# Optimization experiments

Measured on AMD Instinct MI355X. Metric: run time of the kernel, lower is better.

## Reference

```python
import jax, jax.numpy as jnp
import numpy as np

B, S, D, E, H, SL = 4, 2048, 2048, 16, 1024, 1
NUM_SLOTS = E * SL
TEMP = 1.0
TOP_K = 2
EPS = 1e-8


def setup_inputs() -> dict:
    key = jax.random.key(0)
    k0, k1, k2, k3 = jax.random.split(key, 4)
    x = jax.random.normal(k0, (B, S, D), dtype=jnp.float32)
    Wd = jax.random.normal(k1, (NUM_SLOTS, D), dtype=jnp.float32) * 0.02
    W1 = jax.random.normal(k2, (E, D, H), dtype=jnp.float32) * 0.02
    b1 = jnp.zeros((E, H), dtype=jnp.float32)
    W2 = jax.random.normal(k3, (E, H, D), dtype=jnp.float32) * 0.02
    b2 = jnp.zeros((E, D), dtype=jnp.float32)
    return {"x": x, "Wd": Wd, "W1": W1, "b1": b1, "W2": W2, "b2": b2}


def reference(x, Wd, W1, b1, W2, b2):
    lead = x.shape[:-1]
    xf = x.reshape(-1, D)                      # [T, D]
    T = xf.shape[0]

    logits = (xf @ Wd.T) / TEMP                # [T, num_slots]
    dispatch = jax.nn.softmax(logits, axis=0)  # softmax over tokens
    combine = jax.nn.softmax(logits, axis=-1)  # softmax over slots

    # Aggregate tokens into slots, run all experts as one batched GEMM chain.
    slot_in = (dispatch.T @ xf).reshape(E, SL, D)                    # [E, SL, D]
    h = jax.nn.gelu(jnp.einsum('esd,edh->esh', slot_in, W1) + b1[:, None, :],
                    approximate=False)
    slot_out = (jnp.einsum('esh,ehd->esd', h, W2) + b2[:, None, :]).reshape(NUM_SLOTS, D)

    out = (combine @ slot_out).reshape(x.shape)

    # Router stats / losses (eval mode: no EMA update of train_scores).
    expert_weights = combine.reshape(T, E, SL).mean(-1)              # [T, E]
    mean_usage = expert_weights.mean(0)                              # [E]
    p = jax.nn.softmax(Wd.mean(0).reshape(E, -1).mean(-1))
    router_loss = E * jnp.sum(mean_usage * p)

    topk_w, topk_idx = jax.lax.top_k(expert_weights, TOP_K)
    topk_w_norm = topk_w / jnp.clip(topk_w.sum(-1, keepdims=True), EPS)

    gate_weights = expert_weights.reshape(*lead, E)
    routing_entropy = -(gate_weights * jnp.log(gate_weights + EPS)).sum(-1).mean()

    return (out,
            router_loss,
            gate_weights,
            topk_idx.reshape(*lead, TOP_K),
            topk_w_norm.reshape(*lead, TOP_K),
            mean_usage,
            routing_entropy,
            dispatch.reshape(*lead, NUM_SLOTS))
```

## Files before the change

kernel.cpp:

```cpp
#include <hip/hip_runtime.h>
#include <math.h>

#define TTOK 8192
#define DIM  2048
#define NH   1024

#define OFF_PART1   0u
#define OFF_NUM     2097152u
#define OFF_COMBINE 2228224u
#define OFF_CSUM    2359296u
#define OFF_MUSUM   2361344u
#define OFF_ENT     2363392u
#define OFF_PART6   2363520u
#define OFF_SRAW    10752128u
#define OFF_HBUF    10784896u
#define OFF_SLOT    10801280u

#define O_OUT   0u
#define O_LOSS  16777216u
#define O_GATE  16777217u
#define O_TOPI  16908289u
#define O_TOPW  16924673u
#define O_MU    16941057u
#define O_ENTR  16941073u
#define O_DISP  16941074u

__device__ __forceinline__ float wave_sum(float v){
  #pragma unroll
  for (int o=1;o<64;o<<=1) v += __shfl_xor(v,o,64);
  return v;
}

__global__ __launch_bounds__(256) void ka_logits(const float* __restrict__ x,
                                                 const float* __restrict__ Wd,
                                                 float* __restrict__ part1){
  const int tb = blockIdx.x >> 4;
  const int kc = blockIdx.x & 15;
  const int t  = tb*256 + threadIdx.x;
  const float4* __restrict__ xr = (const float4*)(x + (size_t)t*DIM + kc*128);
  float acc[16];
  #pragma unroll
  for (int e=0;e<16;e++) acc[e]=0.f;
  #pragma unroll 4
  for (int k4=0;k4<32;k4++){
    float4 xv = xr[k4];
    #pragma unroll
    for (int e=0;e<16;e++){
      float4 w = *(const float4*)(Wd + e*DIM + kc*128 + k4*4);
      acc[e] += xv.x*w.x + xv.y*w.y + xv.z*w.z + xv.w*w.w;
    }
  }
  float4* po = (float4*)(part1 + ((size_t)kc*TTOK + t)*16);
  po[0] = make_float4(acc[0],acc[1],acc[2],acc[3]);
  po[1] = make_float4(acc[4],acc[5],acc[6],acc[7]);
  po[2] = make_float4(acc[8],acc[9],acc[10],acc[11]);
  po[3] = make_float4(acc[12],acc[13],acc[14],acc[15]);
}

__global__ __launch_bounds__(256) void kb_router(const float* __restrict__ part1,
    float* __restrict__ num, float* __restrict__ csum_part,
    float* __restrict__ combine, float* __restrict__ gate_out,
    float* __restrict__ topi_out, float* __restrict__ topw_out,
    float* __restrict__ musum_part, float* __restrict__ ent_part){
  const int tid = threadIdx.x;
  const int i = blockIdx.x*256 + tid;
  const float4* p1 = (const float4*)part1;
  float4 s = make_float4(0,0,0,0);
  #pragma unroll
  for (int kc=0;kc<16;kc++){
    float4 v = p1[(size_t)kc*32768 + i];
    s.x+=v.x; s.y+=v.y; s.z+=v.z; s.w+=v.w;
  }
  float4 n4 = make_float4(expf(s.x),expf(s.y),expf(s.z),expf(s.w));
  ((float4*)num)[i] = n4;
  __shared__ float Lg[64][20];
  const int tl = tid>>2, q = tid&3;
  *(float4*)(&Lg[tl][q*4]) = s;
  float4 n = n4;
  #pragma unroll
  for (int o=4;o<64;o<<=1){
    n.x += __shfl_xor(n.x,o,64); n.y += __shfl_xor(n.y,o,64);
    n.z += __shfl_xor(n.z,o,64); n.w += __shfl_xor(n.w,o,64);
  }
  __shared__ float4 red[4][4];
  const int w = tid>>6, lane = tid&63;
  if (lane<4) red[w][lane] = n;
  __syncthreads();
  if (tid<4){
    float4 a=red[0][tid],b=red[1][tid],c=red[2][tid],d=red[3][tid];
    *(float4*)(csum_part + blockIdx.x*16 + tid*4) =
      make_float4(a.x+b.x+c.x+d.x, a.y+b.y+c.y+d.y, a.z+b.z+c.z+d.z, a.w+b.w+c.w+d.w);
  }
  if (tid < 64){
    const int gt = blockIdx.x*64 + tid;
    float l[16];
    #pragma unroll
    for (int e=0;e<16;e++) l[e] = Lg[tid][e];
    float m = l[0];
    #pragma unroll
    for (int e=1;e<16;e++) m = fmaxf(m,l[e]);
    float c[16]; float sm=0.f;
    #pragma unroll
    for (int e=0;e<16;e++){ c[e]=expf(l[e]-m); sm+=c[e]; }
    float inv = 1.f/sm;
    #pragma unroll
    for (int e=0;e<16;e++) c[e]*=inv;
    float4* co = (float4*)(combine + (size_t)gt*16);
    co[0]=make_float4(c[0],c[1],c[2],c[3]);   co[1]=make_float4(c[4],c[5],c[6],c[7]);
    co[2]=make_float4(c[8],c[9],c[10],c[11]); co[3]=make_float4(c[12],c[13],c[14],c[15]);
    float* go = gate_out + (size_t)gt*16;
    #pragma unroll
    for (int e=0;e<16;e++) go[e]=c[e];
    float v0=-1.f, v1=-1.f; int i0=0, i1=0;
    #pragma unroll
    for (int e=0;e<16;e++){
      float ce=c[e];
      if (ce>v0){ v1=v0; i1=i0; v0=ce; i0=e; }
      else if (ce>v1){ v1=ce; i1=e; }
    }
    float dn = fmaxf(v0+v1, 1e-8f);
    topi_out[(size_t)gt*2+0]=(float)i0; topi_out[(size_t)gt*2+1]=(float)i1;
    topw_out[(size_t)gt*2+0]=v0/dn;     topw_out[(size_t)gt*2+1]=v1/dn;
    float ent=0.f;
    #pragma unroll
    for (int e=0;e<16;e++) ent -= c[e]*logf(c[e]+1e-8f);
    #pragma unroll
    for (int e=0;e<16;e++){
      float v = wave_sum(c[e]);
      if (tid==0) musum_part[blockIdx.x*16+e] = v;
    }
    float ve = wave_sum(ent);
    if (tid==0) ent_part[blockIdx.x] = ve;
  }
}

__global__ __launch_bounds__(256) void kd_slotin(const float* __restrict__ x,
    const float* __restrict__ num, const float* __restrict__ csum_part,
    const float* __restrict__ musum_part, const float* __restrict__ ent_part,
    const float* __restrict__ Wd,
    float* __restrict__ part6, float* __restrict__ disp_out,
    float* __restrict__ loss_out, float* __restrict__ mu_out, float* __restrict__ ent_out){
  const int tc = blockIdx.x >> 1;
  const int dc = blockIdx.x & 1;
  const int tid = threadIdx.x;
  const int d  = dc*1024 + tid*4;
  const int t0 = tc*32;
  __shared__ float4 sN[128];
  if (tid < 128) sN[tid] = ((const float4*)num)[t0*4 + tid];
  __syncthreads();
  float4 acc[16];
  #pragma unroll
  for (int e=0;e<16;e++) acc[e]=make_float4(0,0,0,0);
  #pragma unroll 2
  for (int t=0;t<32;t++){
    const float4 xv = *(const float4*)(x + (size_t)(t0+t)*DIM + d);
    #pragma unroll
    for (int qq=0;qq<4;qq++){
      float4 nq = sN[t*4+qq];
      acc[qq*4+0].x=fmaf(nq.x,xv.x,acc[qq*4+0].x); acc[qq*4+0].y=fmaf(nq.x,xv.y,acc[qq*4+0].y);
      acc[qq*4+0].z=fmaf(nq.x,xv.z,acc[qq*4+0].z); acc[qq*4+0].w=fmaf(nq.x,xv.w,acc[qq*4+0].w);
      acc[qq*4+1].x=fmaf(nq.y,xv.x,acc[qq*4+1].x); acc[qq*4+1].y=fmaf(nq.y,xv.y,acc[qq*4+1].y);
      acc[qq*4+1].z=fmaf(nq.y,xv.z,acc[qq*4+1].z); acc[qq*4+1].w=fmaf(nq.y,xv.w,acc[qq*4+1].w);
      acc[qq*4+2].x=fmaf(nq.z,xv.x,acc[qq*4+2].x); acc[qq*4+2].y=fmaf(nq.z,xv.y,acc[qq*4+2].y);
      acc[qq*4+2].z=fmaf(nq.z,xv.z,acc[qq*4+2].z); acc[qq*4+2].w=fmaf(nq.z,xv.w,acc[qq*4+2].w);
      acc[qq*4+3].x=fmaf(nq.w,xv.x,acc[qq*4+3].x); acc[qq*4+3].y=fmaf(nq.w,xv.y,acc[qq*4+3].y);
      acc[qq*4+3].z=fmaf(nq.w,xv.z,acc[qq*4+3].z); acc[qq*4+3].w=fmaf(nq.w,xv.w,acc[qq*4+3].w);
    }
  }
  #pragma unroll
  for (int e=0;e<16;e++)
    *(float4*)(part6 + ((size_t)tc*16+e)*DIM + d) = acc[e];

  if (dc==0){
    __shared__ float sIv[16][16];
    __shared__ float sInv[16];
    { int g = tid>>4, e = tid&15;
      float v=0.f;
      #pragma unroll
      for (int k=0;k<8;k++) v += csum_part[(g*8+k)*16 + e];
      sIv[g][e]=v; }
    __syncthreads();
    if (tid<16){
      float v=0.f;
      #pragma unroll
      for (int g2=0;g2<16;g2++) v+=sIv[g2][tid];
      sInv[tid]=1.f/v;
    }
    __syncthreads();
    const float* sNf = (const float*)sN;
    const int j = tid*2;
    float2 dv = make_float2(sNf[j]*sInv[j&15], sNf[j+1]*sInv[(j+1)&15]);
    *(float2*)(disp_out + (size_t)t0*16 + j) = dv;

    if (tc==0){
      __shared__ float sq[16][16];
      __shared__ float smu[16];
      __shared__ float sqv[16];
      __shared__ float sqe[16];
      {
        int s = tid>>4, ch = tid&15;
        const float* base = Wd + (size_t)s*DIM + ch*128;
        float qv=0.f;
        for (int ii=0;ii<128;ii+=4){ float4 v=*(const float4*)(base+ii); qv+=v.x+v.y+v.z+v.w; }
        sq[s][ch]=qv;
      }
      if (tid<16){
        float mu=0.f;
        for (int b=0;b<128;b++) mu += musum_part[b*16+tid];
        mu/=8192.f;
        mu_out[tid]=mu; smu[tid]=mu;
      }
      if (tid==32){ float es=0.f; for(int b=0;b<128;b++) es+=ent_part[b]; ent_out[0]=es/8192.f; }
      __syncthreads();
      if (tid<16){ float qv=0.f; for(int s=0;s<16;s++) qv+=sq[s][tid]; sqv[tid]=qv/2048.f; }
      __syncthreads();
      if (tid<16){
        float qm=-INFINITY;
        for (int e=0;e<16;e++) qm=fmaxf(qm,sqv[e]);
        sqe[tid]=expf(sqv[tid]-qm);
      }
      __syncthreads();
      if (tid==0){
        float qs=0.f; for(int e=0;e<16;e++) qs+=sqe[e];
        float loss=0.f; for(int e=0;e<16;e++) loss+=smu[e]*(sqe[e]/qs);
        loss_out[0]=16.f*loss;
      }
    }
  }
}

__global__ __launch_bounds__(256) void ke_sraw(const float* __restrict__ part6,
    float* __restrict__ sraw){
  const int tid = threadIdx.x;
  const int half = tid>>7, il = tid&127;
  const int i = blockIdx.x*128 + il;
  float s=0.f;
  #pragma unroll 8
  for (int tc=half*128; tc<half*128+128; tc++) s += part6[(size_t)tc*32768 + i];
  __shared__ float s2[256];
  s2[tid]=s;
  __syncthreads();
  if (tid<128){
    int ii = blockIdx.x*128 + tid;
    sraw[ii] = s2[tid]+s2[tid+128];
  }
}

__global__ __launch_bounds__(256) void kf_h(const float* __restrict__ sraw,
    const float* __restrict__ W1, const float* __restrict__ b1,
    const float* __restrict__ csum_part, float* __restrict__ hbuf){
  const int e  = blockIdx.x >> 5;
  const int hc = blockIdx.x & 31;
  const int hbase = hc*32;
  const int tid = threadIdx.x;
  __shared__ float sr[2048];
  __shared__ float sacc[256];
  __shared__ float sIpart[2];
  { const float4* s4 = (const float4*)(sraw + (size_t)e*DIM);
    float4 a = s4[tid*2], b = s4[tid*2+1];
    *(float4*)(&sr[tid*8]) = a; *(float4*)(&sr[tid*8+4]) = b; }
  if (tid < 128){
    float v = csum_part[tid*16 + e];
    #pragma unroll
    for (int o=1;o<64;o<<=1) v += __shfl_xor(v,o,64);
    if ((tid&63)==0) sIpart[tid>>6] = v;
  }
  __syncthreads();
  const int hl = tid&31, ds = tid>>5;
  float acc = 0.f;
  const float* wp = W1 + (size_t)e*DIM*NH + hbase + hl;
  #pragma unroll 16
  for (int d2=0; d2<256; d2++){
    const int dd = d2*8 + ds;
    acc = fmaf(sr[dd], wp[(size_t)dd*NH], acc);
  }
  sacc[tid] = acc;
  __syncthreads();
  if (tid < 32){
    float s = 0.f;
    #pragma unroll
    for (int k=0;k<8;k++) s += sacc[k*32 + tid];
    float invs = 1.f/(sIpart[0]+sIpart[1]);
    float pre = invs*s + b1[(size_t)e*NH + hbase + tid];
    hbuf[(size_t)e*NH + hbase + tid] = 0.5f*pre*(1.f+erff(pre*0.70710678118654752f));
  }
}

__global__ __launch_bounds__(256) void kg_so(const float* __restrict__ hbuf,
    const float* __restrict__ W2, const float* __restrict__ b2,
    float* __restrict__ slot_out){
  const int e  = blockIdx.x >> 5;
  const int dc = blockIdx.x & 31;
  const int dbase = dc*64;
  const int tid = threadIdx.x;
  __shared__ float hh[1024];
  __shared__ float sacc[256];
  { const float4* h4 = (const float4*)(hbuf + (size_t)e*NH);
    *(float4*)(&hh[tid*4]) = h4[tid]; }
  __syncthreads();
  const int dl = tid&63, hs = tid>>6;
  float acc = 0.f;
  const float* wp = W2 + (size_t)e*NH*DIM + dbase + dl;
  #pragma unroll 16
  for (int h2=0; h2<256; h2++){
    const int hidx = h2*4 + hs;
    acc = fmaf(hh[hidx], wp[(size_t)hidx*DIM], acc);
  }
  sacc[tid] = acc;
  __syncthreads();
  if (tid < 64){
    float s = sacc[tid] + sacc[64+tid] + sacc[128+tid] + sacc[192+tid];
    slot_out[(size_t)e*DIM + dbase + tid] = s + b2[(size_t)e*DIM + dbase + tid];
  }
}

__global__ __launch_bounds__(256) void kh_out(const float* __restrict__ slot_out,
    const float* __restrict__ combine, float* __restrict__ out){
  const int tb = blockIdx.x >> 1;
  const int dc = blockIdx.x & 1;
  const int t0 = tb*16;
  const int d  = dc*1024 + threadIdx.x*4;
  float4 sv[16];
  #pragma unroll
  for (int e=0;e<16;e++) sv[e] = *(const float4*)(slot_out + (size_t)e*DIM + d);
  #pragma unroll 2
  for (int t=0;t<16;t++){
    const float* cr = combine + (size_t)(t0+t)*16;
    float4 a = make_float4(0,0,0,0);
    #pragma unroll
    for (int e=0;e<16;e++){
      float c = cr[e];
      a.x=fmaf(c,sv[e].x,a.x); a.y=fmaf(c,sv[e].y,a.y);
      a.z=fmaf(c,sv[e].z,a.z); a.w=fmaf(c,sv[e].w,a.w);
    }
    *(float4*)(out + (size_t)(t0+t)*DIM + d) = a;
  }
}

extern "C" void kernel_launch(void* const* d_in, const int* in_sizes, int n_in,
                              void* d_out, int out_size, void* d_ws, size_t ws_size,
                              hipStream_t stream) {
  const float* x  = (const float*)d_in[0];
  const float* Wd = (const float*)d_in[1];
  const float* W1 = (const float*)d_in[2];
  const float* b1 = (const float*)d_in[3];
  const float* W2 = (const float*)d_in[4];
  const float* b2 = (const float*)d_in[5];
  float* out = (float*)d_out;
  float* ws  = (float*)d_ws;

  float* part1   = ws + OFF_PART1;
  float* num     = ws + OFF_NUM;
  float* combine = ws + OFF_COMBINE;
  float* csump   = ws + OFF_CSUM;
  float* musump  = ws + OFF_MUSUM;
  float* entp    = ws + OFF_ENT;
  float* part6   = ws + OFF_PART6;
  float* sraw    = ws + OFF_SRAW;
  float* hbuf    = ws + OFF_HBUF;
  float* slot_out= ws + OFF_SLOT;

  ka_logits<<<512, 256, 0, stream>>>(x, Wd, part1);
  kb_router<<<128, 256, 0, stream>>>(part1, num, csump, combine, out + O_GATE,
                                     out + O_TOPI, out + O_TOPW, musump, entp);
  kd_slotin<<<512, 256, 0, stream>>>(x, num, csump, musump, entp, Wd,
                                     part6, out + O_DISP, out + O_LOSS,
                                     out + O_MU, out + O_ENTR);
  ke_sraw<<<256, 256, 0, stream>>>(part6, sraw);
  kf_h<<<512, 256, 0, stream>>>(sraw, W1, b1, csump, hbuf);
  kg_so<<<512, 256, 0, stream>>>(hbuf, W2, b2, slot_out);
  kh_out<<<1024, 256, 0, stream>>>(slot_out, combine, out + O_OUT);
}
```

Before: 179.2 us.

## Repartition logits, W1 and W2 GEMV kernels into finer splits with more blocks

The logits kernel now splits the reduction dimension into 64 chunks of 32 and has each thread handle two tokens, which reuses each Wd load twice. The router now sums 64 partials instead of 16. The two expert GEMV kernels double their block counts by narrowing the column tile and switching to contiguous per-thread row ranges. The workspace is laid out again so that part1, which has grown to 64 partials, reuses the part6 region. The aim is more parallelism for the memory-bound GEMVs. The cost is more partial-sum traffic and less coalesced column access for the narrower tiles.

New measurement: 203.8 us. 13.7% more time.

```diff
diff --git a/kernel.cpp b/kernel.cpp
--- a/kernel.cpp
+++ b/kernel.cpp
@@ -6,15 +6,15 @@
 #define NH   1024
 
 #define OFF_PART1   0u
-#define OFF_NUM     2097152u
-#define OFF_COMBINE 2228224u
-#define OFF_CSUM    2359296u
-#define OFF_MUSUM   2361344u
-#define OFF_ENT     2363392u
-#define OFF_PART6   2363520u
-#define OFF_SRAW    10752128u
-#define OFF_HBUF    10784896u
-#define OFF_SLOT    10801280u
+#define OFF_PART6   0u
+#define OFF_NUM     8388608u
+#define OFF_COMBINE 8519680u
+#define OFF_CSUM    8650752u
+#define OFF_MUSUM   8652800u
+#define OFF_ENT     8654848u
+#define OFF_SRAW    8654976u
+#define OFF_HBUF    8687744u
+#define OFF_SLOT    8704128u
 
 #define O_OUT   0u
 #define O_LOSS  16777216u
@@ -34,27 +34,31 @@
 __global__ __launch_bounds__(256) void ka_logits(const float* __restrict__ x,
                                                  const float* __restrict__ Wd,
                                                  float* __restrict__ part1){
-  const int tb = blockIdx.x >> 4;
-  const int kc = blockIdx.x & 15;
-  const int t  = tb*256 + threadIdx.x;
-  const float4* __restrict__ xr = (const float4*)(x + (size_t)t*DIM + kc*128);
-  float acc[16];
-  #pragma unroll
-  for (int e=0;e<16;e++) acc[e]=0.f;
-  #pragma unroll 4
-  for (int k4=0;k4<32;k4++){
-    float4 xv = xr[k4];
+  const int tb = blockIdx.x >> 6;
+  const int kc = blockIdx.x & 63;
+  const int t0 = tb*512 + threadIdx.x;
+  const float4* __restrict__ xr0 = (const float4*)(x + (size_t)t0*DIM + kc*32);
+  const float4* __restrict__ xr1 = (const float4*)(x + (size_t)(t0+256)*DIM + kc*32);
+  float a0[16], a1[16];
+  #pragma unroll
+  for (int e=0;e<16;e++){ a0[e]=0.f; a1[e]=0.f; }
+  #pragma unroll
+  for (int k4=0;k4<8;k4++){
+    float4 x0 = xr0[k4];
+    float4 x1 = xr1[k4];
     #pragma unroll
     for (int e=0;e<16;e++){
-      float4 w = *(const float4*)(Wd + e*DIM + kc*128 + k4*4);
-      acc[e] += xv.x*w.x + xv.y*w.y + xv.z*w.z + xv.w*w.w;
-    }
-  }
-  float4* po = (float4*)(part1 + ((size_t)kc*TTOK + t)*16);
-  po[0] = make_float4(acc[0],acc[1],acc[2],acc[3]);
-  po[1] = make_float4(acc[4],acc[5],acc[6],acc[7]);
-  po[2] = make_float4(acc[8],acc[9],acc[10],acc[11]);
-  po[3] = make_float4(acc[12],acc[13],acc[14],acc[15]);
+      float4 w = *(const float4*)(Wd + e*DIM + kc*32 + k4*4);
+      a0[e] += x0.x*w.x + x0.y*w.y + x0.z*w.z + x0.w*w.w;
+      a1[e] += x1.x*w.x + x1.y*w.y + x1.z*w.z + x1.w*w.w;
+    }
+  }
+  float4* p0 = (float4*)(part1 + ((size_t)kc*TTOK + t0)*16);
+  p0[0]=make_float4(a0[0],a0[1],a0[2],a0[3]);   p0[1]=make_float4(a0[4],a0[5],a0[6],a0[7]);
+  p0[2]=make_float4(a0[8],a0[9],a0[10],a0[11]); p0[3]=make_float4(a0[12],a0[13],a0[14],a0[15]);
+  float4* p1 = (float4*)(part1 + ((size_t)kc*TTOK + t0+256)*16);
+  p1[0]=make_float4(a1[0],a1[1],a1[2],a1[3]);   p1[1]=make_float4(a1[4],a1[5],a1[6],a1[7]);
+  p1[2]=make_float4(a1[8],a1[9],a1[10],a1[11]); p1[3]=make_float4(a1[12],a1[13],a1[14],a1[15]);
 }
 
 __global__ __launch_bounds__(256) void kb_router(const float* __restrict__ part1,
@@ -66,8 +70,8 @@
   const int i = blockIdx.x*256 + tid;
   const float4* p1 = (const float4*)part1;
   float4 s = make_float4(0,0,0,0);
-  #pragma unroll
-  for (int kc=0;kc<16;kc++){
+  #pragma unroll 8
+  for (int kc=0;kc<64;kc++){
     float4 v = p1[(size_t)kc*32768 + i];
     s.x+=v.x; s.y+=v.y; s.z+=v.z; s.w+=v.w;
   }
@@ -249,9 +253,9 @@
 __global__ __launch_bounds__(256) void kf_h(const float* __restrict__ sraw,
     const float* __restrict__ W1, const float* __restrict__ b1,
     const float* __restrict__ csum_part, float* __restrict__ hbuf){
-  const int e  = blockIdx.x >> 5;
-  const int hc = blockIdx.x & 31;
-  const int hbase = hc*32;
+  const int e  = blockIdx.x >> 6;
+  const int hc = blockIdx.x & 63;
+  const int hbase = hc*16;
   const int tid = threadIdx.x;
   __shared__ float sr[2048];
   __shared__ float sacc[256];
@@ -266,20 +270,20 @@
     if ((tid&63)==0) sIpart[tid>>6] = v;
   }
   __syncthreads();
-  const int hl = tid&31, ds = tid>>5;
+  const int hl = tid&15, ds = tid>>4;
   float acc = 0.f;
   const float* wp = W1 + (size_t)e*DIM*NH + hbase + hl;
   #pragma unroll 16
-  for (int d2=0; d2<256; d2++){
-    const int dd = d2*8 + ds;
+  for (int i=0;i<128;i++){
+    const int dd = ds*128 + i;
     acc = fmaf(sr[dd], wp[(size_t)dd*NH], acc);
   }
   sacc[tid] = acc;
   __syncthreads();
-  if (tid < 32){
+  if (tid < 16){
     float s = 0.f;
     #pragma unroll
-    for (int k=0;k<8;k++) s += sacc[k*32 + tid];
+    for (int k=0;k<16;k++) s += sacc[k*16 + tid];
     float invs = 1.f/(sIpart[0]+sIpart[1]);
     float pre = invs*s + b1[(size_t)e*NH + hbase + tid];
     hbuf[(size_t)e*NH + hbase + tid] = 0.5f*pre*(1.f+erff(pre*0.70710678118654752f));
@@ -289,27 +293,29 @@
 __global__ __launch_bounds__(256) void kg_so(const float* __restrict__ hbuf,
     const float* __restrict__ W2, const float* __restrict__ b2,
     float* __restrict__ slot_out){
-  const int e  = blockIdx.x >> 5;
-  const int dc = blockIdx.x & 31;
-  const int dbase = dc*64;
+  const int e  = blockIdx.x >> 6;
+  const int dc = blockIdx.x & 63;
+  const int dbase = dc*32;
   const int tid = threadIdx.x;
   __shared__ float hh[1024];
   __shared__ float sacc[256];
   { const float4* h4 = (const float4*)(hbuf + (size_t)e*NH);
     *(float4*)(&hh[tid*4]) = h4[tid]; }
   __syncthreads();
-  const int dl = tid&63, hs = tid>>6;
+  const int dl = tid&31, hs = tid>>5;
   float acc = 0.f;
   const float* wp = W2 + (size_t)e*NH*DIM + dbase + dl;
   #pragma unroll 16
-  for (int h2=0; h2<256; h2++){
-    const int hidx = h2*4 + hs;
+  for (int i=0;i<128;i++){
+    const int hidx = hs*128 + i;
     acc = fmaf(hh[hidx], wp[(size_t)hidx*DIM], acc);
   }
   sacc[tid] = acc;
   __syncthreads();
-  if (tid < 64){
-    float s = sacc[tid] + sacc[64+tid] + sacc[128+tid] + sacc[192+tid];
+  if (tid < 32){
+    float s = 0.f;
+    #pragma unroll
+    for (int k=0;k<8;k++) s += sacc[k*32 + tid];
     slot_out[(size_t)e*DIM + dbase + tid] = s + b2[(size_t)e*DIM + dbase + tid];
   }
 }
@@ -360,14 +366,14 @@
   float* hbuf    = ws + OFF_HBUF;
   float* slot_out= ws + OFF_SLOT;
 
-  ka_logits<<<512, 256, 0, stream>>>(x, Wd, part1);
+  ka_logits<<<1024, 256, 0, stream>>>(x, Wd, part1);
   kb_router<<<128, 256, 0, stream>>>(part1, num, csump, combine, out + O_GATE,
                                      out + O_TOPI, out + O_TOPW, musump, entp);
   kd_slotin<<<512, 256, 0, stream>>>(x, num, csump, musump, entp, Wd,
                                      part6, out + O_DISP, out + O_LOSS,
                                      out + O_MU, out + O_ENTR);
   ke_sraw<<<256, 256, 0, stream>>>(part6, sraw);
-  kf_h<<<512, 256, 0, stream>>>(sraw, W1, b1, csump, hbuf);
-  kg_so<<<512, 256, 0, stream>>>(hbuf, W2, b2, slot_out);
+  kf_h<<<1024, 256, 0, stream>>>(sraw, W1, b1, csump, hbuf);
+  kg_so<<<1024, 256, 0, stream>>>(hbuf, W2, b2, slot_out);
   kh_out<<<1024, 256, 0, stream>>>(slot_out, combine, out + O_OUT);
 }
```

## Fuse logits, router, and slot aggregation into one kernel; merge reductions

Applied to the files above, without the earlier changes.

Merges the logits GEMV, the router softmax/top-k/entropy, and the token-to-slot aggregation into a single 512-thread kernel per 32-token chunk. Each x row is then read while it is likely still in cache, and the part1 partial-logit buffer round trip goes away. The part6 reduction is merged with the dispatch normalisation, loss, usage and entropy finalisation into one kernel that pre-scales sraw by the inverse column sums, so kf_h no longer recomputes them. Launch count drops from seven to five. In exchange the fused kernel has only 256 blocks and heavy register use, which may lower occupancy.

Measured after the change: 213.9 us. 1.19x slower.

```diff
diff --git a/kernel.cpp b/kernel.cpp
--- a/kernel.cpp
+++ b/kernel.cpp
@@ -5,16 +5,15 @@
 #define DIM  2048
 #define NH   1024
 
-#define OFF_PART1   0u
-#define OFF_NUM     2097152u
-#define OFF_COMBINE 2228224u
-#define OFF_CSUM    2359296u
-#define OFF_MUSUM   2361344u
-#define OFF_ENT     2363392u
-#define OFF_PART6   2363520u
-#define OFF_SRAW    10752128u
-#define OFF_HBUF    10784896u
-#define OFF_SLOT    10801280u
+#define OFF_PART6 0u
+#define OFF_NUM   8388608u
+#define OFF_COMB  8519680u
+#define OFF_CSUM  8650752u
+#define OFF_MUSUM 8654848u
+#define OFF_ENT   8658944u
+#define OFF_SRAW  8659200u
+#define OFF_HBUF  8691968u
+#define OFF_SLOT  8708352u
 
 #define O_OUT   0u
 #define O_LOSS  16777216u
@@ -25,77 +24,62 @@
 #define O_ENTR  16941073u
 #define O_DISP  16941074u
 
-__device__ __forceinline__ float wave_sum(float v){
-  #pragma unroll
-  for (int o=1;o<64;o<<=1) v += __shfl_xor(v,o,64);
-  return v;
-}
-
-__global__ __launch_bounds__(256) void ka_logits(const float* __restrict__ x,
-                                                 const float* __restrict__ Wd,
-                                                 float* __restrict__ part1){
-  const int tb = blockIdx.x >> 4;
-  const int kc = blockIdx.x & 15;
-  const int t  = tb*256 + threadIdx.x;
-  const float4* __restrict__ xr = (const float4*)(x + (size_t)t*DIM + kc*128);
-  float acc[16];
-  #pragma unroll
-  for (int e=0;e<16;e++) acc[e]=0.f;
-  #pragma unroll 4
-  for (int k4=0;k4<32;k4++){
-    float4 xv = xr[k4];
-    #pragma unroll
-    for (int e=0;e<16;e++){
-      float4 w = *(const float4*)(Wd + e*DIM + kc*128 + k4*4);
-      acc[e] += xv.x*w.x + xv.y*w.y + xv.z*w.z + xv.w*w.w;
-    }
-  }
-  float4* po = (float4*)(part1 + ((size_t)kc*TTOK + t)*16);
-  po[0] = make_float4(acc[0],acc[1],acc[2],acc[3]);
-  po[1] = make_float4(acc[4],acc[5],acc[6],acc[7]);
-  po[2] = make_float4(acc[8],acc[9],acc[10],acc[11]);
-  po[3] = make_float4(acc[12],acc[13],acc[14],acc[15]);
-}
-
-__global__ __launch_bounds__(256) void kb_router(const float* __restrict__ part1,
-    float* __restrict__ num, float* __restrict__ csum_part,
-    float* __restrict__ combine, float* __restrict__ gate_out,
+__global__ __launch_bounds__(512) void kad(const float* __restrict__ x,
+    const float* __restrict__ Wd,
+    float* __restrict__ num, float* __restrict__ comb, float* __restrict__ gate_out,
     float* __restrict__ topi_out, float* __restrict__ topw_out,
-    float* __restrict__ musum_part, float* __restrict__ ent_part){
+    float* __restrict__ csum_p, float* __restrict__ musum_p, float* __restrict__ ent_p,
+    float* __restrict__ part6){
+  const int blk = blockIdx.x;
   const int tid = threadIdx.x;
-  const int i = blockIdx.x*256 + tid;
-  const float4* p1 = (const float4*)part1;
-  float4 s = make_float4(0,0,0,0);
-  #pragma unroll
-  for (int kc=0;kc<16;kc++){
-    float4 v = p1[(size_t)kc*32768 + i];
-    s.x+=v.x; s.y+=v.y; s.z+=v.z; s.w+=v.w;
-  }
-  float4 n4 = make_float4(expf(s.x),expf(s.y),expf(s.z),expf(s.w));
-  ((float4*)num)[i] = n4;
-  __shared__ float Lg[64][20];
-  const int tl = tid>>2, q = tid&3;
-  *(float4*)(&Lg[tl][q*4]) = s;
-  float4 n = n4;
-  #pragma unroll
-  for (int o=4;o<64;o<<=1){
-    n.x += __shfl_xor(n.x,o,64); n.y += __shfl_xor(n.y,o,64);
-    n.z += __shfl_xor(n.z,o,64); n.w += __shfl_xor(n.w,o,64);
-  }
-  __shared__ float4 red[4][4];
-  const int w = tid>>6, lane = tid&63;
-  if (lane<4) red[w][lane] = n;
-  __syncthreads();
-  if (tid<4){
-    float4 a=red[0][tid],b=red[1][tid],c=red[2][tid],d=red[3][tid];
-    *(float4*)(csum_part + blockIdx.x*16 + tid*4) =
-      make_float4(a.x+b.x+c.x+d.x, a.y+b.y+c.y+d.y, a.z+b.z+c.z+d.z, a.w+b.w+c.w+d.w);
-  }
-  if (tid < 64){
-    const int gt = blockIdx.x*64 + tid;
+  const int t0  = blk*32;
+  __shared__ float sS[32][17];
+  __shared__ __align__(16) float sN[32][16];
+  __shared__ float sC[32][16];
+  __shared__ float sE[32];
+
+  {
+    const int ttp = tid>>5;
+    const int kc  = tid&31;
+    const float4* xr0 = (const float4*)(x + (size_t)(t0+2*ttp  )*DIM + kc*64);
+    const float4* xr1 = (const float4*)(x + (size_t)(t0+2*ttp+1)*DIM + kc*64);
+    float a0[16], a1[16];
+    #pragma unroll
+    for (int e=0;e<16;e++){ a0[e]=0.f; a1[e]=0.f; }
+    #pragma unroll
+    for (int k4=0;k4<16;k4++){
+      float4 x0 = xr0[k4];
+      float4 x1 = xr1[k4];
+      #pragma unroll
+      for (int e=0;e<16;e++){
+        float4 w = *(const float4*)(Wd + e*DIM + kc*64 + k4*4);
+        a0[e] += x0.x*w.x + x0.y*w.y + x0.z*w.z + x0.w*w.w;
+        a1[e] += x1.x*w.x + x1.y*w.y + x1.z*w.z + x1.w*w.w;
+      }
+    }
+    #pragma unroll
+    for (int o=1;o<32;o<<=1){
+      #pragma unroll
+      for (int e=0;e<16;e++){
+        a0[e] += __shfl_xor(a0[e],o,64);
+        a1[e] += __shfl_xor(a1[e],o,64);
+      }
+    }
+    if (kc==0){
+      #pragma unroll
+      for (int e=0;e<16;e++){
+        sS[2*ttp  ][e] = a0[e];  sN[2*ttp  ][e] = expf(a0[e]);
+        sS[2*ttp+1][e] = a1[e];  sN[2*ttp+1][e] = expf(a1[e]);
+      }
+    }
+  }
+  __syncthreads();
+  if (tid<128) ((float4*)num)[(size_t)blk*128 + tid] = ((const float4*)sN)[tid];
+  if (tid<32){
+    const int gt = t0 + tid;
     float l[16];
     #pragma unroll
-    for (int e=0;e<16;e++) l[e] = Lg[tid][e];
+    for (int e=0;e<16;e++) l[e] = sS[tid][e];
     float m = l[0];
     #pragma unroll
     for (int e=1;e<16;e++) m = fmaxf(m,l[e]);
@@ -105,166 +89,158 @@
     float inv = 1.f/sm;
     #pragma unroll
     for (int e=0;e<16;e++) c[e]*=inv;
-    float4* co = (float4*)(combine + (size_t)gt*16);
+    float4* co = (float4*)(comb + (size_t)gt*16);
     co[0]=make_float4(c[0],c[1],c[2],c[3]);   co[1]=make_float4(c[4],c[5],c[6],c[7]);
     co[2]=make_float4(c[8],c[9],c[10],c[11]); co[3]=make_float4(c[12],c[13],c[14],c[15]);
     float* go = gate_out + (size_t)gt*16;
     #pragma unroll
     for (int e=0;e<16;e++) go[e]=c[e];
-    float v0=-1.f, v1=-1.f; int i0=0, i1=0;
+    float v0=-1.f,v1=-1.f; int i0=0,i1=0;
     #pragma unroll
     for (int e=0;e<16;e++){
       float ce=c[e];
-      if (ce>v0){ v1=v0; i1=i0; v0=ce; i0=e; }
-      else if (ce>v1){ v1=ce; i1=e; }
-    }
-    float dn = fmaxf(v0+v1, 1e-8f);
+      if (ce>v0){ v1=v0;i1=i0; v0=ce;i0=e; }
+      else if (ce>v1){ v1=ce;i1=e; }
+    }
+    float dn = fmaxf(v0+v1,1e-8f);
     topi_out[(size_t)gt*2+0]=(float)i0; topi_out[(size_t)gt*2+1]=(float)i1;
     topw_out[(size_t)gt*2+0]=v0/dn;     topw_out[(size_t)gt*2+1]=v1/dn;
     float ent=0.f;
     #pragma unroll
     for (int e=0;e<16;e++) ent -= c[e]*logf(c[e]+1e-8f);
-    #pragma unroll
-    for (int e=0;e<16;e++){
-      float v = wave_sum(c[e]);
-      if (tid==0) musum_part[blockIdx.x*16+e] = v;
-    }
-    float ve = wave_sum(ent);
-    if (tid==0) ent_part[blockIdx.x] = ve;
-  }
-}
-
-__global__ __launch_bounds__(256) void kd_slotin(const float* __restrict__ x,
-    const float* __restrict__ num, const float* __restrict__ csum_part,
-    const float* __restrict__ musum_part, const float* __restrict__ ent_part,
+    sE[tid]=ent;
+    #pragma unroll
+    for (int e=0;e<16;e++) sC[tid][e]=c[e];
+  }
+  __syncthreads();
+  if (tid<16){
+    float ms=0.f, cs=0.f;
+    #pragma unroll
+    for (int tt=0;tt<32;tt++){ ms += sC[tt][tid]; cs += sN[tt][tid]; }
+    musum_p[blk*16+tid]=ms; csum_p[blk*16+tid]=cs;
+  }
+  if (tid==16){
+    float s=0.f;
+    #pragma unroll
+    for (int k=0;k<32;k++) s += sE[k];
+    ent_p[blk]=s;
+  }
+  __syncthreads();
+  {
+    float4 acc[16];
+    #pragma unroll
+    for (int e=0;e<16;e++) acc[e]=make_float4(0,0,0,0);
+    #pragma unroll 2
+    for (int t=0;t<32;t++){
+      const float4 xv = *(const float4*)(x + (size_t)(t0+t)*DIM + tid*4);
+      #pragma unroll
+      for (int qq=0;qq<4;qq++){
+        float4 nq = *((const float4*)&sN[t][qq*4]);
+        acc[qq*4+0].x=fmaf(nq.x,xv.x,acc[qq*4+0].x); acc[qq*4+0].y=fmaf(nq.x,xv.y,acc[qq*4+0].y);
+        acc[qq*4+0].z=fmaf(nq.x,xv.z,acc[qq*4+0].z); acc[qq*4+0].w=fmaf(nq.x,xv.w,acc[qq*4+0].w);
+        acc[qq*4+1].x=fmaf(nq.y,xv.x,acc[qq*4+1].x); acc[qq*4+1].y=fmaf(nq.y,xv.y,acc[qq*4+1].y);
+        acc[qq*4+1].z=fmaf(nq.y,xv.z,acc[qq*4+1].z); acc[qq*4+1].w=fmaf(nq.y,xv.w,acc[qq*4+1].w);
+        acc[qq*4+2].x=fmaf(nq.z,xv.x,acc[qq*4+2].x); acc[qq*4+2].y=fmaf(nq.z,xv.y,acc[qq*4+2].y);
+        acc[qq*4+2].z=fmaf(nq.z,xv.z,acc[qq*4+2].z); acc[qq*4+2].w=fmaf(nq.z,xv.w,acc[qq*4+2].w);
+        acc[qq*4+3].x=fmaf(nq.w,xv.x,acc[qq*4+3].x); acc[qq*4+3].y=fmaf(nq.w,xv.y,acc[qq*4+3].y);
+        acc[qq*4+3].z=fmaf(nq.w,xv.z,acc[qq*4+3].z); acc[qq*4+3].w=fmaf(nq.w,xv.w,acc[qq*4+3].w);
+      }
+    }
+    #pragma unroll
+    for (int e=0;e<16;e++)
+      *(float4*)(part6 + ((size_t)blk*16+e)*DIM + tid*4) = acc[e];
+  }
+}
+
+__global__ __launch_bounds__(256) void ke2(const float* __restrict__ part6,
+    const float* __restrict__ csum_p, const float* __restrict__ num,
+    const float* __restrict__ musum_p, const float* __restrict__ ent_p,
     const float* __restrict__ Wd,
-    float* __restrict__ part6, float* __restrict__ disp_out,
+    float* __restrict__ sraw, float* __restrict__ disp_out,
     float* __restrict__ loss_out, float* __restrict__ mu_out, float* __restrict__ ent_out){
-  const int tc = blockIdx.x >> 1;
-  const int dc = blockIdx.x & 1;
-  const int tid = threadIdx.x;
-  const int d  = dc*1024 + tid*4;
-  const int t0 = tc*32;
-  __shared__ float4 sN[128];
-  if (tid < 128) sN[tid] = ((const float4*)num)[t0*4 + tid];
-  __syncthreads();
-  float4 acc[16];
-  #pragma unroll
-  for (int e=0;e<16;e++) acc[e]=make_float4(0,0,0,0);
-  #pragma unroll 2
-  for (int t=0;t<32;t++){
-    const float4 xv = *(const float4*)(x + (size_t)(t0+t)*DIM + d);
-    #pragma unroll
-    for (int qq=0;qq<4;qq++){
-      float4 nq = sN[t*4+qq];
-      acc[qq*4+0].x=fmaf(nq.x,xv.x,acc[qq*4+0].x); acc[qq*4+0].y=fmaf(nq.x,xv.y,acc[qq*4+0].y);
-      acc[qq*4+0].z=fmaf(nq.x,xv.z,acc[qq*4+0].z); acc[qq*4+0].w=fmaf(nq.x,xv.w,acc[qq*4+0].w);
-      acc[qq*4+1].x=fmaf(nq.y,xv.x,acc[qq*4+1].x); acc[qq*4+1].y=fmaf(nq.y,xv.y,acc[qq*4+1].y);
-      acc[qq*4+1].z=fmaf(nq.y,xv.z,acc[qq*4+1].z); acc[qq*4+1].w=fmaf(nq.y,xv.w,acc[qq*4+1].w);
-      acc[qq*4+2].x=fmaf(nq.z,xv.x,acc[qq*4+2].x); acc[qq*4+2].y=fmaf(nq.z,xv.y,acc[qq*4+2].y);
-      acc[qq*4+2].z=fmaf(nq.z,xv.z,acc[qq*4+2].z); acc[qq*4+2].w=fmaf(nq.z,xv.w,acc[qq*4+2].w);
-      acc[qq*4+3].x=fmaf(nq.w,xv.x,acc[qq*4+3].x); acc[qq*4+3].y=fmaf(nq.w,xv.y,acc[qq*4+3].y);
-      acc[qq*4+3].z=fmaf(nq.w,xv.z,acc[qq*4+3].z); acc[qq*4+3].w=fmaf(nq.w,xv.w,acc[qq*4+3].w);
-    }
-  }
-  #pragma unroll
-  for (int e=0;e<16;e++)
-    *(float4*)(part6 + ((size_t)tc*16+e)*DIM + d) = acc[e];
-
-  if (dc==0){
-    __shared__ float sIv[16][16];
-    __shared__ float sInv[16];
-    { int g = tid>>4, e = tid&15;
-      float v=0.f;
-      #pragma unroll
-      for (int k=0;k<8;k++) v += csum_part[(g*8+k)*16 + e];
-      sIv[g][e]=v; }
+  const int tid = threadIdx.x, blk = blockIdx.x;
+  __shared__ float sIv[16][16];
+  __shared__ float sInv[16];
+  __shared__ float s2[256];
+  { int g=tid>>4, e=tid&15;
+    float v=0.f;
+    #pragma unroll
+    for (int k=0;k<16;k++) v += csum_p[(g*16+k)*16 + e];
+    sIv[g][e]=v; }
+  __syncthreads();
+  if (tid<16){
+    float v=0.f;
+    #pragma unroll
+    for (int g=0;g<16;g++) v += sIv[g][tid];
+    sInv[tid]=1.f/v;
+  }
+  __syncthreads();
+  { const int ol=tid&31, sl=tid>>5;
+    const int o = blk*32 + ol;
+    float s=0.f;
+    #pragma unroll 8
+    for (int k=0;k<32;k++) s += part6[(size_t)(sl*32+k)*32768 + o];
+    s2[tid]=s;
+  }
+  __syncthreads();
+  if (tid<32){
+    float t=0.f;
+    #pragma unroll
+    for (int k=0;k<8;k++) t += s2[k*32+tid];
+    const int oo = blk*32 + tid;
+    sraw[oo] = t * sInv[oo>>11];
+  }
+  if (blk<512){
+    const int t0 = blk*16;
+    float v = num[(size_t)t0*16 + tid];
+    disp_out[(size_t)t0*16 + tid] = v * sInv[tid&15];
+  }
+  if (blk==1023){
+    __shared__ float sq[16][16];
+    __shared__ float smu[16];
+    __shared__ float sqv[16];
+    __shared__ float sqe[16];
+    { int s=tid>>4, ch=tid&15;
+      const float* base = Wd + (size_t)s*DIM + ch*128;
+      float qv=0.f;
+      for (int ii=0;ii<128;ii+=4){ float4 v=*(const float4*)(base+ii); qv+=v.x+v.y+v.z+v.w; }
+      sq[s][ch]=qv; }
+    if (tid<16){
+      float mu=0.f;
+      for (int b=0;b<256;b++) mu += musum_p[b*16+tid];
+      mu/=8192.f;
+      mu_out[tid]=mu; smu[tid]=mu;
+    }
+    if (tid==32){ float es=0.f; for(int b=0;b<256;b++) es+=ent_p[b]; ent_out[0]=es/8192.f; }
+    __syncthreads();
+    if (tid<16){ float qv=0.f; for(int s=0;s<16;s++) qv+=sq[s][tid]; sqv[tid]=qv/2048.f; }
     __syncthreads();
     if (tid<16){
-      float v=0.f;
-      #pragma unroll
-      for (int g2=0;g2<16;g2++) v+=sIv[g2][tid];
-      sInv[tid]=1.f/v;
+      float qm=-INFINITY;
+      for (int e=0;e<16;e++) qm=fmaxf(qm,sqv[e]);
+      sqe[tid]=expf(sqv[tid]-qm);
     }
     __syncthreads();
-    const float* sNf = (const float*)sN;
-    const int j = tid*2;
-    float2 dv = make_float2(sNf[j]*sInv[j&15], sNf[j+1]*sInv[(j+1)&15]);
-    *(float2*)(disp_out + (size_t)t0*16 + j) = dv;
-
-    if (tc==0){
-      __shared__ float sq[16][16];
-      __shared__ float smu[16];
-      __shared__ float sqv[16];
-      __shared__ float sqe[16];
-      {
-        int s = tid>>4, ch = tid&15;
-        const float* base = Wd + (size_t)s*DIM + ch*128;
-        float qv=0.f;
-        for (int ii=0;ii<128;ii+=4){ float4 v=*(const float4*)(base+ii); qv+=v.x+v.y+v.z+v.w; }
-        sq[s][ch]=qv;
-      }
-      if (tid<16){
-        float mu=0.f;
-        for (int b=0;b<128;b++) mu += musum_part[b*16+tid];
-        mu/=8192.f;
-        mu_out[tid]=mu; smu[tid]=mu;
-      }
-      if (tid==32){ float es=0.f; for(int b=0;b<128;b++) es+=ent_part[b]; ent_out[0]=es/8192.f; }
-      __syncthreads();
-      if (tid<16){ float qv=0.f; for(int s=0;s<16;s++) qv+=sq[s][tid]; sqv[tid]=qv/2048.f; }
-      __syncthreads();
-      if (tid<16){
-        float qm=-INFINITY;
-        for (int e=0;e<16;e++) qm=fmaxf(qm,sqv[e]);
-        sqe[tid]=expf(sqv[tid]-qm);
-      }
-      __syncthreads();
-      if (tid==0){
-        float qs=0.f; for(int e=0;e<16;e++) qs+=sqe[e];
-        float loss=0.f; for(int e=0;e<16;e++) loss+=smu[e]*(sqe[e]/qs);
-        loss_out[0]=16.f*loss;
-      }
-    }
-  }
-}
-
-__global__ __launch_bounds__(256) void ke_sraw(const float* __restrict__ part6,
-    float* __restrict__ sraw){
-  const int tid = threadIdx.x;
-  const int half = tid>>7, il = tid&127;
-  const int i = blockIdx.x*128 + il;
-  float s=0.f;
-  #pragma unroll 8
-  for (int tc=half*128; tc<half*128+128; tc++) s += part6[(size_t)tc*32768 + i];
-  __shared__ float s2[256];
-  s2[tid]=s;
-  __syncthreads();
-  if (tid<128){
-    int ii = blockIdx.x*128 + tid;
-    sraw[ii] = s2[tid]+s2[tid+128];
+    if (tid==0){
+      float qs=0.f; for(int e=0;e<16;e++) qs+=sqe[e];
+      float loss=0.f; for(int e=0;e<16;e++) loss+=smu[e]*(sqe[e]/qs);
+      loss_out[0]=16.f*loss;
+    }
   }
 }
 
 __global__ __launch_bounds__(256) void kf_h(const float* __restrict__ sraw,
     const float* __restrict__ W1, const float* __restrict__ b1,
-    const float* __restrict__ csum_part, float* __restrict__ hbuf){
+    float* __restrict__ hbuf){
   const int e  = blockIdx.x >> 5;
   const int hc = blockIdx.x & 31;
   const int hbase = hc*32;
   const int tid = threadIdx.x;
   __shared__ float sr[2048];
   __shared__ float sacc[256];
-  __shared__ float sIpart[2];
   { const float4* s4 = (const float4*)(sraw + (size_t)e*DIM);
     float4 a = s4[tid*2], b = s4[tid*2+1];
     *(float4*)(&sr[tid*8]) = a; *(float4*)(&sr[tid*8+4]) = b; }
-  if (tid < 128){
-    float v = csum_part[tid*16 + e];
-    #pragma unroll
-    for (int o=1;o<64;o<<=1) v += __shfl_xor(v,o,64);
-    if ((tid&63)==0) sIpart[tid>>6] = v;
-  }
   __syncthreads();
   const int hl = tid&31, ds = tid>>5;
   float acc = 0.f;
@@ -280,8 +256,7 @@
     float s = 0.f;
     #pragma unroll
     for (int k=0;k<8;k++) s += sacc[k*32 + tid];
-    float invs = 1.f/(sIpart[0]+sIpart[1]);
-    float pre = invs*s + b1[(size_t)e*NH + hbase + tid];
+    float pre = s + b1[(size_t)e*NH + hbase + tid];
     hbuf[(size_t)e*NH + hbase + tid] = 0.5f*pre*(1.f+erff(pre*0.70710678118654752f));
   }
 }
@@ -349,25 +324,22 @@
   float* out = (float*)d_out;
   float* ws  = (float*)d_ws;
 
-  float* part1   = ws + OFF_PART1;
-  float* num     = ws + OFF_NUM;
-  float* combine = ws + OFF_COMBINE;
-  float* csump   = ws + OFF_CSUM;
-  float* musump  = ws + OFF_MUSUM;
-  float* entp    = ws + OFF_ENT;
-  float* part6   = ws + OFF_PART6;
-  float* sraw    = ws + OFF_SRAW;
-  float* hbuf    = ws + OFF_HBUF;
-  float* slot_out= ws + OFF_SLOT;
-
-  ka_logits<<<512, 256, 0, stream>>>(x, Wd, part1);
-  kb_router<<<128, 256, 0, stream>>>(part1, num, csump, combine, out + O_GATE,
-                                     out + O_TOPI, out + O_TOPW, musump, entp);
-  kd_slotin<<<512, 256, 0, stream>>>(x, num, csump, musump, entp, Wd,
-                                     part6, out + O_DISP, out + O_LOSS,
-                                     out + O_MU, out + O_ENTR);
-  ke_sraw<<<256, 256, 0, stream>>>(part6, sraw);
-  kf_h<<<512, 256, 0, stream>>>(sraw, W1, b1, csump, hbuf);
-  kg_so<<<512, 256, 0, stream>>>(hbuf, W2, b2, slot_out);
-  kh_out<<<1024, 256, 0, stream>>>(slot_out, combine, out + O_OUT);
-}
+  float* part6 = ws + OFF_PART6;
+  float* num   = ws + OFF_NUM;
+  float* comb  = ws + OFF_COMB;
+  float* csump = ws + OFF_CSUM;
+  float* musump= ws + OFF_MUSUM;
+  float* entp  = ws + OFF_ENT;
+  float* sraw  = ws + OFF_SRAW;
+  float* hbuf  = ws + OFF_HBUF;
+  float* slot  = ws + OFF_SLOT;
+
+  kad<<<256, 512, 0, stream>>>(x, Wd, num, comb, out + O_GATE, out + O_TOPI,
+                               out + O_TOPW, csump, musump, entp, part6);
+  ke2<<<1024, 256, 0, stream>>>(part6, csump, num, musump, entp, Wd,
+                                sraw, out + O_DISP, out + O_LOSS,
+                                out + O_MU, out + O_ENTR);
+  kf_h<<<512, 256, 0, stream>>>(sraw, W1, b1, hbuf);
+  kg_so<<<512, 256, 0, stream>>>(hbuf, W2, b2, slot);
+  kh_out<<<1024, 256, 0, stream>>>(slot, comb, out + O_OUT);
+}
```
